# Kernel optimization log

Hardware: AMD Instinct MI355X
Metric: run time of the kernel (lower is better)

Reference implementation:

```python
import jax, jax.numpy as jnp
import numpy as np

B, IC, HW = 16, 32, 128
NF, OC, K, GROUP = 8, 64, 5, 8


def _rotate_filters(w, theta):
    """Bilinear rotation of filters w [N, C, k, k] by angle theta.
    Matches torch affine_grid + grid_sample (align_corners=False, zero padding)."""
    k = w.shape[-1]
    base = (2.0 * jnp.arange(k, dtype=w.dtype) + 1.0) / k - 1.0  # pixel-center normalized coords
    ys, xs = jnp.meshgrid(base, base, indexing='ij')  # [k, k]
    c, s = jnp.cos(theta), jnp.sin(theta)
    # sampling grid = rot_mat @ [x, y, 1]
    gx = c * xs - s * ys
    gy = s * xs + c * ys
    # normalized -> pixel coords (align_corners=False)
    ix = ((gx + 1.0) * k - 1.0) / 2.0
    iy = ((gy + 1.0) * k - 1.0) / 2.0
    x0 = jnp.floor(ix)
    y0 = jnp.floor(iy)
    wx1 = ix - x0
    wy1 = iy - y0
    wx0 = 1.0 - wx1
    wy0 = 1.0 - wy1

    def gather(yy, xx):
        valid = ((xx >= 0) & (xx < k) & (yy >= 0) & (yy < k)).astype(w.dtype)
        xc = jnp.clip(xx, 0, k - 1).astype(jnp.int32)
        yc = jnp.clip(yy, 0, k - 1).astype(jnp.int32)
        return w[:, :, yc, xc] * valid  # [N, C, k, k]

    return (gather(y0, x0) * (wy0 * wx0)
            + gather(y0, x0 + 1.0) * (wy0 * wx1)
            + gather(y0 + 1.0, x0) * (wy1 * wx0)
            + gather(y0 + 1.0, x0 + 1.0) * (wy1 * wx1))


def _forward(x, kernel, relaxed_weights):
    nf, oc, ic, k, _ = kernel.shape
    group = relaxed_weights.shape[1]
    wflat = kernel.reshape(nf * oc, ic, k, k)
    thetas = -2.0 * jnp.pi / group * jnp.arange(group, dtype=x.dtype)
    # [group, nf*oc, ic, k, k]
    fb = jax.vmap(lambda t: _rotate_filters(wflat, t))(thetas)
    # -> [nf, oc, group, ic, k, k]
    fb = jnp.transpose(fb, (1, 0, 2, 3, 4)).reshape(nf, oc, group, ic, k, k)
    w = jnp.einsum('na,noaikl->oaikl', relaxed_weights, fb)
    w = w.reshape(oc * group, ic, k, k)
    pad = (k - 1) // 2
    y = jax.lax.conv_general_dilated(
        x, w, window_strides=(1, 1), padding=[(pad, pad), (pad, pad)],
        dimension_numbers=('NCHW', 'OIHW', 'NCHW'))
    b, _, h, wd = y.shape
    y = y.reshape(b, oc, group, wd, h)  # matches torch .view(B, O, A, W, H)
    return jax.nn.leaky_relu(y, negative_slope=0.01)


def setup_inputs() -> dict:
    key = jax.random.key(0)
    k1, k2, k3 = jax.random.split(key, 3)
    x = jax.random.normal(k1, (B, IC, HW, HW), dtype=jnp.float32)
    kernel = jax.random.normal(k2, (NF, OC, IC, K, K), dtype=jnp.float32) * 0.05
    relaxed_weights = jax.random.normal(k3, (NF, GROUP), dtype=jnp.float32)
    return {"x": x, "kernel": kernel, "relaxed_weights": relaxed_weights}


def reference(x, kernel, relaxed_weights):
    return _forward(x, kernel, relaxed_weights)
```

## Files before the change

### kernel.cpp

```cpp
#include <hip/hip_runtime.h>
#include <hip/hip_bf16.h>
#include <math.h>

#define B_   16
#define IC_  32
#define HW_  128
#define NF_  8
#define OC_  64
#define K_   5
#define GRP_ 8
#define COTOT_ (OC_ * GRP_)
#define XTH  132

typedef short  short8  __attribute__((ext_vector_type(8)));
typedef unsigned short ushort8 __attribute__((ext_vector_type(8)));
typedef float  f32x4   __attribute__((ext_vector_type(4)));

static __device__ inline unsigned short f2bf(float f) {
    unsigned u = __builtin_bit_cast(unsigned, f);
    unsigned r = (u + 0x7FFFu + ((u >> 16) & 1u)) >> 16;
    return (unsigned short)r;
}

__device__ __forceinline__ void gload16(void* lds, const void* g) {
    __builtin_amdgcn_global_load_lds(
        (const __attribute__((address_space(1))) unsigned int*)g,
        (__attribute__((address_space(3))) unsigned int*)lds, 16, 0, 0);
}

__global__ __launch_bounds__(256) void xform_kernel(
    const float* __restrict__ x, unsigned short* __restrict__ xt) {
    int idx = blockIdx.x * blockDim.x + threadIdx.x;
    const int TOT = B_ * XTH * XTH;
    if (idx >= TOT) return;
    int wp = idx % XTH;
    int t  = idx / XTH;
    int hp = t % XTH;
    int b  = t / XTH;

    unsigned short vals[IC_];
    bool interior = (hp >= 2) && (hp < 2 + HW_) && (wp >= 2) && (wp < 2 + HW_);
    if (interior) {
        const float* xb = x + ((size_t)b * IC_) * (HW_ * HW_) + (hp - 2) * HW_ + (wp - 2);
        #pragma unroll
        for (int ic = 0; ic < IC_; ++ic)
            vals[ic] = f2bf(xb[(size_t)ic * (HW_ * HW_)]);
    } else {
        #pragma unroll
        for (int ic = 0; ic < IC_; ++ic) vals[ic] = 0;
    }
    ushort8* dst = (ushort8*)(xt + (size_t)idx * IC_);
    #pragma unroll
    for (int c = 0; c < 4; ++c) {
        ushort8 v;
        #pragma unroll
        for (int j = 0; j < 8; ++j) v[j] = vals[c * 8 + j];
        dst[c] = v;
    }
}

__global__ __launch_bounds__(256) void build_w_kernel(
    const float* __restrict__ kern,
    const float* __restrict__ relaxed,
    unsigned short* __restrict__ wt) {
    int idx = blockIdx.x * blockDim.x + threadIdx.x;
    const int TOT = 25 * COTOT_ * IC_;
    if (idx >= TOT) return;
    int ic = idx & (IC_ - 1);
    int t  = idx >> 5;
    int co = t & (COTOT_ - 1);
    int e  = t >> 9;
    int a  = co & (GRP_ - 1);
    int o  = co >> 3;
    int i  = e / K_;
    int j  = e - i * K_;

    float theta = -6.283185307179586f / (float)GRP_ * (float)a;
    float cth = cosf(theta), sth = sinf(theta);
    float bx = (2.0f * (float)j + 1.0f) / (float)K_ - 1.0f;
    float by = (2.0f * (float)i + 1.0f) / (float)K_ - 1.0f;
    float gx = cth * bx - sth * by;
    float gy = sth * bx + cth * by;
    float ix = ((gx + 1.0f) * (float)K_ - 1.0f) * 0.5f;
    float iy = ((gy + 1.0f) * (float)K_ - 1.0f) * 0.5f;
    float x0 = floorf(ix), y0 = floorf(iy);
    float wx1 = ix - x0, wy1 = iy - y0;
    float wx0 = 1.0f - wx1, wy0 = 1.0f - wy1;

    float xs2[2]  = {x0, x0 + 1.0f};
    float ys2[2]  = {y0, y0 + 1.0f};
    float wxs[2] = {wx0, wx1};
    float wys[2] = {wy0, wy1};

    float tw[4];
    int   tyc[4], txc[4];
    #pragma unroll
    for (int dy = 0; dy < 2; ++dy) {
        #pragma unroll
        for (int dx = 0; dx < 2; ++dx) {
            float xx = xs2[dx], yy = ys2[dy];
            bool valid = (xx >= 0.0f) && (xx < (float)K_) &&
                         (yy >= 0.0f) && (yy < (float)K_);
            int tp = dy * 2 + dx;
            tw[tp]  = wys[dy] * wxs[dx] * (valid ? 1.0f : 0.0f);
            txc[tp] = (int)fminf(fmaxf(xx, 0.0f), (float)(K_ - 1));
            tyc[tp] = (int)fminf(fmaxf(yy, 0.0f), (float)(K_ - 1));
        }
    }

    float acc = 0.0f;
    #pragma unroll
    for (int n = 0; n < NF_; ++n) {
        const float* kb = kern + ((size_t)((n * OC_ + o) * IC_ + ic)) * (K_ * K_);
        float v = 0.0f;
        #pragma unroll
        for (int tp = 0; tp < 4; ++tp)
            v += kb[tyc[tp] * K_ + txc[tp]] * tw[tp];
        acc += relaxed[n * GRP_ + a] * v;
    }
    wt[idx] = f2bf(acc);
}

__global__ __launch_bounds__(256, 2) void conv_mfma_kernel(
    const unsigned short* __restrict__ xt,
    const unsigned short* __restrict__ wt,
    float* __restrict__ out) {
    __shared__ __align__(16) unsigned short xs[4 * 6 * XTH * 8];
    __shared__ __align__(16) unsigned short wbuf[2][4 * 128 * 8];

    int tid  = threadIdx.x;
    int lane = tid & 63;
    int wv   = tid >> 6;
    int l15  = lane & 15;
    int l4   = lane >> 4;
    int hr   = wv >> 1;
    int wn   = wv & 1;

    int cg = blockIdx.x;
    int hp = blockIdx.y;
    int b  = blockIdx.z;
    int cobase = cg * 128;
    int h0 = hp * 2;

    {
        const unsigned short* xb = xt + (((size_t)b * XTH + h0) * XTH) * IC_;
        for (int i = 0; i < 13; ++i) {
            int s = i * 256 + tid;
            if (s < 3168) {
                int ch  = s / (6 * XTH);
                int rem = s - ch * (6 * XTH);
                int row = rem / XTH;
                int w   = rem - row * XTH;
                gload16(&xs[s * 8], xb + ((size_t)row * XTH + w) * IC_ + ch * 8);
            }
        }
    }
    {
        const unsigned short* wsrc = wt + (size_t)cobase * IC_;
        #pragma unroll
        for (int i = 0; i < 2; ++i) {
            int s  = i * 256 + tid;
            int ch = s >> 7;
            int co = s & 127;
            gload16(&wbuf[0][s * 8], wsrc + (size_t)co * IC_ + ch * 8);
        }
    }
    __syncthreads();

    f32x4 acc[8][4];
    #pragma unroll
    for (int m = 0; m < 8; ++m)
        #pragma unroll
        for (int n = 0; n < 4; ++n) acc[m][n] = (f32x4)(0.0f);

    for (int t = 0; t < 25; ++t) {
        int bi = t & 1;
        if (t < 24) {
            const unsigned short* wsrc = wt + ((size_t)(t + 1) * COTOT_ + cobase) * IC_;
            #pragma unroll
            for (int i = 0; i < 2; ++i) {
                int s  = i * 256 + tid;
                int ch = s >> 7;
                int co = s & 127;
                gload16(&wbuf[bi ^ 1][s * 8], wsrc + (size_t)co * IC_ + ch * 8);
            }
        }
        int ky = t / 5;
        int kx = t - ky * 5;
        int row = hr + ky;

        short8 af[8], bf[4];
        #pragma unroll
        for (int m = 0; m < 8; ++m)
            af[m] = *(const short8*)&wbuf[bi][(l4 * 128 + m * 16 + l15) * 8];
        #pragma unroll
        for (int n = 0; n < 4; ++n)
            bf[n] = *(const short8*)&xs[((l4 * 6 + row) * XTH +
                                        (wn * 64 + n * 16 + l15 + kx)) * 8];
        #pragma unroll
        for (int m = 0; m < 8; ++m)
            #pragma unroll
            for (int n = 0; n < 4; ++n)
                acc[m][n] = __builtin_amdgcn_mfma_f32_16x16x32_bf16(
                    af[m], bf[n], acc[m][n], 0, 0, 0);

        __syncthreads();
    }

    int h = h0 + hr;
    float* ob = out + ((size_t)b * COTOT_ + cobase) * (HW_ * HW_)
                    + (size_t)h * HW_ + wn * 64;
    #pragma unroll
    for (int m = 0; m < 8; ++m) {
        #pragma unroll
        for (int n = 0; n < 4; ++n) {
            #pragma unroll
            for (int r = 0; r < 4; ++r) {
                int co = m * 16 + l4 * 4 + r;
                int w  = n * 16 + l15;
                float v = acc[m][n][r];
                v = (v >= 0.0f) ? v : 0.01f * v;
                ob[(size_t)co * (HW_ * HW_) + w] = v;
            }
        }
    }
}

extern "C" void kernel_launch(void* const* d_in, const int* in_sizes, int n_in,
                              void* d_out, int out_size, void* d_ws, size_t ws_size,
                              hipStream_t stream) {
    const float* x       = (const float*)d_in[0];
    const float* kernel  = (const float*)d_in[1];
    const float* relaxed = (const float*)d_in[2];
    float* out = (float*)d_out;

    unsigned short* xt = (unsigned short*)d_ws;
    unsigned short* wt = (unsigned short*)((char*)d_ws + (size_t)B_ * XTH * XTH * IC_ * 2);

    const int xtot = B_ * XTH * XTH;
    xform_kernel<<<(xtot + 255) / 256, 256, 0, stream>>>(x, xt);

    const int wtot = 25 * COTOT_ * IC_;
    build_w_kernel<<<(wtot + 255) / 256, 256, 0, stream>>>(kernel, relaxed, wt);

    dim3 grid(COTOT_ / 128, HW_ / 2, B_);
    conv_mfma_kernel<<<grid, 256, 0, stream>>>(xt, wt, out);
}
```

Before: 269.7 us.

## Load conv weights directly into registers with double buffering, drop LDS weight staging

Weight fragments are now read straight from global memory into two register sets that alternate per tap, instead of being staged through a double-buffered LDS array. This removes the per-tap __syncthreads and the LDS round trip for weights, and fully unrolls the tap loop. The grid order is also changed so that blocks sharing the same output-channel group run together, which may improve L2 reuse of weights. The cost is higher register pressure from 16 extra short8 fragments and redundant global weight loads across waves.

```diff
diff --git a/kernel.cpp b/kernel.cpp
--- a/kernel.cpp
+++ b/kernel.cpp
@@ -11,6 +11,7 @@
 #define GRP_ 8
 #define COTOT_ (OC_ * GRP_)
 #define XTH  132
+#define TAPSTRIDE (COTOT_ * IC_)
 
 typedef short  short8  __attribute__((ext_vector_type(8)));
 typedef unsigned short ushort8 __attribute__((ext_vector_type(8)));
@@ -126,7 +127,6 @@
     const unsigned short* __restrict__ wt,
     float* __restrict__ out) {
     __shared__ __align__(16) unsigned short xs[4 * 6 * XTH * 8];
-    __shared__ __align__(16) unsigned short wbuf[2][4 * 128 * 8];
 
     int tid  = threadIdx.x;
     int lane = tid & 63;
@@ -136,9 +136,9 @@
     int hr   = wv >> 1;
     int wn   = wv & 1;
 
-    int cg = blockIdx.x;
-    int hp = blockIdx.y;
-    int b  = blockIdx.z;
+    int hp = blockIdx.x;
+    int b  = blockIdx.y;
+    int cg = blockIdx.z;
     int cobase = cg * 128;
     int h0 = hp * 2;
 
@@ -155,56 +155,60 @@
             }
         }
     }
-    {
-        const unsigned short* wsrc = wt + (size_t)cobase * IC_;
-        #pragma unroll
-        for (int i = 0; i < 2; ++i) {
-            int s  = i * 256 + tid;
-            int ch = s >> 7;
-            int co = s & 127;
-            gload16(&wbuf[0][s * 8], wsrc + (size_t)co * IC_ + ch * 8);
-        }
-    }
+
+    const unsigned short* wl = wt + (size_t)(cobase + l15) * IC_ + l4 * 8;
+
+    short8 af0[8], af1[8];
+    #pragma unroll
+    for (int m = 0; m < 8; ++m)
+        af0[m] = *(const short8*)(wl + (size_t)m * 16 * IC_);
+
+    f32x4 acc[8][4];
+    #pragma unroll
+    for (int m = 0; m < 8; ++m)
+        #pragma unroll
+        for (int n = 0; n < 4; ++n) acc[m][n] = (f32x4)(0.0f);
+
     __syncthreads();
 
-    f32x4 acc[8][4];
-    #pragma unroll
-    for (int m = 0; m < 8; ++m)
-        #pragma unroll
-        for (int n = 0; n < 4; ++n) acc[m][n] = (f32x4)(0.0f);
-
+    #pragma unroll
     for (int t = 0; t < 25; ++t) {
-        int bi = t & 1;
         if (t < 24) {
-            const unsigned short* wsrc = wt + ((size_t)(t + 1) * COTOT_ + cobase) * IC_;
-            #pragma unroll
-            for (int i = 0; i < 2; ++i) {
-                int s  = i * 256 + tid;
-                int ch = s >> 7;
-                int co = s & 127;
-                gload16(&wbuf[bi ^ 1][s * 8], wsrc + (size_t)co * IC_ + ch * 8);
+            const unsigned short* wn_ = wl + (size_t)(t + 1) * TAPSTRIDE;
+            if (t & 1) {
+                #pragma unroll
+                for (int m = 0; m < 8; ++m)
+                    af0[m] = *(const short8*)(wn_ + (size_t)m * 16 * IC_);
+            } else {
+                #pragma unroll
+                for (int m = 0; m < 8; ++m)
+                    af1[m] = *(const short8*)(wn_ + (size_t)m * 16 * IC_);
             }
         }
-        int ky = t / 5;
-        int kx = t - ky * 5;
-        int row = hr + ky;
-
-        short8 af[8], bf[4];
-        #pragma unroll
-        for (int m = 0; m < 8; ++m)
-            af[m] = *(const short8*)&wbuf[bi][(l4 * 128 + m * 16 + l15) * 8];
+        const int ky = t / 5;
+        const int kx = t - ky * 5;
+        const int row = hr + ky;
+
+        short8 bf[4];
         #pragma unroll
         for (int n = 0; n < 4; ++n)
             bf[n] = *(const short8*)&xs[((l4 * 6 + row) * XTH +
                                         (wn * 64 + n * 16 + l15 + kx)) * 8];
-        #pragma unroll
-        for (int m = 0; m < 8; ++m)
+        if (t & 1) {
             #pragma unroll
-            for (int n = 0; n < 4; ++n)
-                acc[m][n] = __builtin_amdgcn_mfma_f32_16x16x32_bf16(
-                    af[m], bf[n], acc[m][n], 0, 0, 0);
-
-        __syncthreads();
+            for (int m = 0; m < 8; ++m)
+                #pragma unroll
+                for (int n = 0; n < 4; ++n)
+                    acc[m][n] = __builtin_amdgcn_mfma_f32_16x16x32_bf16(
+                        af1[m], bf[n], acc[m][n], 0, 0, 0);
+        } else {
+            #pragma unroll
+            for (int m = 0; m < 8; ++m)
+                #pragma unroll
+                for (int n = 0; n < 4; ++n)
+                    acc[m][n] = __builtin_amdgcn_mfma_f32_16x16x32_bf16(
+                        af0[m], bf[n], acc[m][n], 0, 0, 0);
+        }
     }
 
     int h = h0 + hr;
@@ -243,6 +247,6 @@
     const int wtot = 25 * COTOT_ * IC_;
     build_w_kernel<<<(wtot + 255) / 256, 256, 0, stream>>>(kernel, relaxed, wt);
 
-    dim3 grid(COTOT_ / 128, HW_ / 2, B_);
+    dim3 grid(HW_ / 2, B_, COTOT_ / 128);
     conv_mfma_kernel<<<grid, 256, 0, stream>>>(xt, wt, out);
 }
```

Measured after the change: 283.9 us. 1.05x slower.
